# Performance work log

Measured on AMD Instinct MI355X. Metric: run time of the kernel, lower is better.

Reference implementation:

```python
import jax, jax.numpy as jnp
import numpy as np

HEADS = 8
DIM_HEAD = 32
HTK = 576
WTK = 576


def layernorm(x, g, b, eps=1e-6):
    mu = x.mean(-1, keepdims=True)
    var = ((x - mu) ** 2).mean(-1, keepdims=True)
    return (x - mu) * jax.lax.rsqrt(var + eps) * g + b


def conv2d(x, w, b, pad, groups=1):
    y = jax.lax.conv_general_dilated(
        x, w, (1, 1), [(pad, pad), (pad, pad)],
        dimension_numbers=('NCHW', 'OIHW', 'NCHW'),
        feature_group_count=groups)
    return y + b[None, :, None, None]


def prune_attn(attn, htk, wtk):
    B, H, N, _ = attn.shape
    bi = jnp.arange(B)[:, None, None]
    hi = jnp.arange(H)[None, :, None]
    # row pruning: score rows by mean over keys, keep top-k rows
    row_scores = attn.mean(-1)                       # [B,H,N]
    _, top_row = jax.lax.top_k(row_scores, htk)      # [B,H,htk]
    row_mask = jnp.zeros((B, H, N), attn.dtype).at[bi, hi, top_row].set(1.0)
    # col pruning: score cols by mean over queries, keep top-k cols
    col_scores = attn.mean(-2)                       # [B,H,N]
    _, top_col = jax.lax.top_k(col_scores, wtk)
    col_mask = jnp.zeros((B, H, N), attn.dtype).at[bi, hi, top_col].set(1.0)
    return attn * row_mask[..., :, None] * col_mask[..., None, :]


def setup_inputs() -> dict:
    key = jax.random.key(0)
    ks = jax.random.split(key, 24)
    C = 256
    hid = C * 4
    g = C // 8
    s = 0.02
    inp = {
        'x': jax.random.normal(ks[0], (2, C, 48, 48), jnp.float32),
        'qkv_w': jax.random.normal(ks[1], (C, 3 * C), jnp.float32) * s,
        'out_w': jax.random.normal(ks[2], (C, C), jnp.float32) * s,
        'ln1_g': jnp.ones((C,), jnp.float32),
        'ln1_b': jnp.zeros((C,), jnp.float32),
        'ln2_g': jnp.ones((C,), jnp.float32),
        'ln2_b': jnp.zeros((C,), jnp.float32),
        'dw_w': jax.random.normal(ks[3], (C, 1, 3, 3), jnp.float32) * s,
        'dw_b': jnp.zeros((C,), jnp.float32),
        'pw_w': jax.random.normal(ks[4], (C, C, 1, 1), jnp.float32) * s,
        'pw_b': jnp.zeros((C,), jnp.float32),
        'sg1_w': jax.random.normal(ks[5], (g, C, 1, 1), jnp.float32) * s,
        'sg1_b': jnp.zeros((g,), jnp.float32),
        'sg2_w': jax.random.normal(ks[6], (1, g, 7, 7), jnp.float32) * s,
        'sg2_b': jnp.zeros((1,), jnp.float32),
        'cg1_w': jax.random.normal(ks[7], (g, C, 1, 1), jnp.float32) * s,
        'cg1_b': jnp.zeros((g,), jnp.float32),
        'cg2_w': jax.random.normal(ks[8], (C, g, 1, 1), jnp.float32) * s,
        'cg2_b': jnp.zeros((C,), jnp.float32),
        'ff_w1': jax.random.normal(ks[9], (C, hid), jnp.float32) * s,
        'ff_b1': jnp.zeros((hid,), jnp.float32),
        'ff_w2': jax.random.normal(ks[10], (hid, C), jnp.float32) * s,
        'ff_b2': jnp.zeros((C,), jnp.float32),
        'gamma1': jnp.full((1,), 0.5, jnp.float32),
        'gamma2': jnp.full((1,), 0.5, jnp.float32),
    }
    return inp


def reference(x, qkv_w, out_w, ln1_g, ln1_b, ln2_g, ln2_b, dw_w, dw_b,
              pw_w, pw_b, sg1_w, sg1_b, sg2_w, sg2_b, cg1_w, cg1_b,
              cg2_w, cg2_b, ff_w1, ff_b1, ff_w2, ff_b2, gamma1, gamma2):
    B, C, H, W = x.shape
    N = H * W
    # ---- dual-pruned self-attention branch ----
    xa = x.transpose(0, 2, 3, 1).reshape(B, N, C)
    xa = layernorm(xa, ln1_g, ln1_b)
    qkv = xa @ qkv_w                                    # [B,N,3C]
    q, k, v = jnp.split(qkv, 3, axis=-1)
    rs = lambda t: t.reshape(B, N, HEADS, DIM_HEAD).transpose(0, 2, 1, 3)
    q, k, v = rs(q), rs(k), rs(v)                       # [B,h,N,d]
    attn = jnp.einsum('bhid,bhjd->bhij', q, k) * (DIM_HEAD ** -0.5)
    attn = prune_attn(attn, HTK, WTK)
    attn = jax.nn.softmax(attn, axis=-1)
    o = jnp.einsum('bhij,bhjd->bhid', attn, v)
    o = o.transpose(0, 2, 1, 3).reshape(B, N, C) @ out_w
    x_attn = o.reshape(B, H, W, C).transpose(0, 3, 1, 2)
    # ---- conv branch ----
    xc = conv2d(x, dw_w, dw_b, pad=1, groups=C)
    xc = conv2d(xc, pw_w, pw_b, pad=0)
    xs = x_attn + xc
    # ---- gates ----
    sg = jax.nn.silu(conv2d(xs, sg1_w, sg1_b, pad=0))
    sg = jax.nn.sigmoid(conv2d(sg, sg2_w, sg2_b, pad=3))   # [B,1,H,W]
    cg = xs.mean(axis=(2, 3), keepdims=True)                # [B,C,1,1]
    cg = jax.nn.silu(conv2d(cg, cg1_w, cg1_b, pad=0))
    cg = jax.nn.sigmoid(conv2d(cg, cg2_w, cg2_b, pad=0))
    x2 = x + gamma1[0] * (xs * sg * cg)
    # ---- FFN ----
    normed = layernorm(x2.transpose(0, 2, 3, 1), ln2_g, ln2_b)
    h = jax.nn.gelu(normed @ ff_w1 + ff_b1, approximate=False)
    ff = (h @ ff_w2 + ff_b2).transpose(0, 3, 1, 2)
    return x2 + gamma2[0] * ff
```

## Files before the change

kernel.cpp:

```cpp
#include <hip/hip_runtime.h>
#include <math.h>

#define N_PIX 2304
#define CCH   256
#define BHN   16
#define KTOP  576
#define NROWS 4608

typedef unsigned short u16;
typedef __attribute__((ext_vector_type(8))) short short8v;
typedef __attribute__((ext_vector_type(4))) float floatx4;

__device__ __forceinline__ u16 f2b(float f) {
  unsigned int u = __float_as_uint(f);
  return (u16)((u + 0x7fffu + ((u >> 16) & 1u)) >> 16);
}
__device__ __forceinline__ float b2f(u16 v) {
  return __uint_as_float(((unsigned int)v) << 16);
}

__device__ __forceinline__ void async16(const void* g, void* l) {
  __builtin_amdgcn_global_load_lds(
      (const __attribute__((address_space(1))) unsigned int*)g,
      (__attribute__((address_space(3))) unsigned int*)l, 16, 0, 0);
}

__device__ __forceinline__ float erf_apx(float x) {
  float ax = fabsf(x);
  float u = 1.f / (1.f + 0.3275911f * ax);
  float y = u * (0.254829592f + u * (-0.284496736f + u * (1.421413741f +
            u * (-1.453152027f + u * 1.061405429f))));
  float r = 1.f - y * expf(-ax * ax);
  return (x < 0.f) ? -r : r;
}

__global__ __launch_bounds__(256) void lncast_kernel(
    const float* __restrict__ x, u16* __restrict__ xa_bf, float* __restrict__ xnhwc,
    const float* __restrict__ g, const float* __restrict__ beta,
    const float* __restrict__ qkv_w, const float* __restrict__ out_w,
    const float* __restrict__ pw_w, const float* __restrict__ ff_w1,
    const float* __restrict__ ff_w2, const float* __restrict__ sg1_w,
    u16* __restrict__ qkvBT, u16* __restrict__ outBT, u16* __restrict__ pwBT,
    u16* __restrict__ ff1BT, u16* __restrict__ ff2BT, u16* __restrict__ sg1BT)
{
  __shared__ float tile[32 * 257];
  __shared__ float redS[8 * 32], redQ[8 * 32];
  __shared__ float mu_s[32], rs_s[32];
  int tid = threadIdx.x;
  if (blockIdx.x >= 144) {
    int i = (blockIdx.x - 144) * 256 + tid;
    if (i < 196608) { int k = i / 768, n = i - k * 768; qkvBT[n * 256 + k] = f2b(qkv_w[i]); return; }
    i -= 196608;
    if (i < 65536) { int k = i >> 8, n = i & 255; outBT[n * 256 + k] = f2b(out_w[i]); return; }
    i -= 65536;
    if (i < 65536) { pwBT[i] = f2b(pw_w[i]); return; }
    i -= 65536;
    if (i < 262144) { int k = i >> 10, n = i & 1023; ff1BT[n * 256 + k] = f2b(ff_w1[i]); return; }
    i -= 262144;
    if (i < 262144) { int k = i & 1023, n = i >> 10; ff2BT[i] = f2b(ff_w2[k * 256 + n]); return; }
    i -= 262144;
    if (i < 16384) sg1BT[i] = (i < 8192) ? f2b(sg1_w[i]) : (u16)0;
    return;
  }
  int p0g = blockIdx.x * 32;
  int bb = p0g / N_PIX; int p0 = p0g - bb * N_PIX;
  int px = tid & 31, csub = tid >> 5;
  float sacc = 0.f, qacc = 0.f;
#pragma unroll 4
  for (int it = 0; it < 32; ++it) {
    int c = it * 8 + csub;
    float v = x[((long)bb * 256 + c) * N_PIX + p0 + px];
    tile[px * 257 + c] = v;
    sacc += v; qacc += v * v;
  }
  redS[csub * 32 + px] = sacc; redQ[csub * 32 + px] = qacc;
  __syncthreads();
  if (tid < 32) {
    float s = 0.f, qq = 0.f;
#pragma unroll
    for (int j = 0; j < 8; ++j) { s += redS[j * 32 + tid]; qq += redQ[j * 32 + tid]; }
    float mu = s * (1.f / 256.f);
    float var = qq * (1.f / 256.f) - mu * mu;
    mu_s[tid] = mu; rs_s[tid] = rsqrtf(var + 1e-6f);
  }
  __syncthreads();
  float gv = g[tid], bv = beta[tid];
#pragma unroll 4
  for (int it = 0; it < 32; ++it) {
    float v = tile[it * 257 + tid];
    long orow = (long)(p0g + it) * 256 + tid;
    xnhwc[orow] = v;
    xa_bf[orow] = f2b((v - mu_s[it]) * rs_s[it] * gv + bv);
  }
}

template<int MT, int EPI, int CS>
__global__ __launch_bounds__(256) void mgemm(
    const u16* __restrict__ A, const u16* __restrict__ BT,
    float* __restrict__ C, u16* __restrict__ C2,
    int K, int ldc, int nvalid,
    const float* __restrict__ bias, const float* __restrict__ add,
    const float* __restrict__ gamma,
    float* __restrict__ cs_out, int cs_ld)
{
  __shared__ u16 Als[MT * 64 * 32];
  __shared__ u16 Bls[64 * 32];
  int tid = threadIdx.x;
  int w = tid >> 6, lane = tid & 63;
  int row0 = blockIdx.y * (MT * 64), col0 = blockIdx.x * 64;
  const u16* Abase = A + (long)row0 * K;
  const u16* Bbase = BT + (long)col0 * K;
  int q = lane >> 4, l15 = lane & 15;

  floatx4 acc[MT][4];
#pragma unroll
  for (int mi = 0; mi < MT; ++mi)
#pragma unroll
    for (int ni = 0; ni < 4; ++ni) acc[mi][ni] = (floatx4)0.f;

  int ccB = w * 64 + lane;
  int rB = ccB >> 2, kB = (ccB & 3) << 3;

  for (int k0 = 0; k0 < K; k0 += 32) {
#pragma unroll
    for (int i = 0; i < MT; ++i) {
      int cc = w * (64 * MT) + i * 64 + lane;
      async16(Abase + (long)(cc >> 2) * K + k0 + ((cc & 3) << 3), &Als[cc * 8]);
    }
    async16(Bbase + (long)rB * K + k0 + kB, &Bls[ccB * 8]);
    __syncthreads();
    short8v a[MT];
#pragma unroll
    for (int mi = 0; mi < MT; ++mi)
      a[mi] = *(const short8v*)&Als[(w * (16 * MT) + mi * 16 + l15) * 32 + q * 8];
#pragma unroll
    for (int ni = 0; ni < 4; ++ni) {
      short8v b = *(const short8v*)&Bls[(ni * 16 + l15) * 32 + q * 8];
#pragma unroll
      for (int mi = 0; mi < MT; ++mi)
        acc[mi][ni] = __builtin_amdgcn_mfma_f32_16x16x32_bf16(a[mi], b, acc[mi][ni], 0, 0, 0);
    }
    __syncthreads();
  }

  float g2 = (EPI == 5) ? gamma[0] : 0.f;
  float cp[4] = {0.f, 0.f, 0.f, 0.f};
#pragma unroll
  for (int mi = 0; mi < MT; ++mi) {
#pragma unroll
    for (int ni = 0; ni < 4; ++ni) {
      int c = col0 + ni * 16 + l15;
      int rbase = row0 + w * (16 * MT) + mi * 16 + q * 4;
#pragma unroll
      for (int reg = 0; reg < 4; ++reg) {
        long row = rbase + reg;
        float v = acc[mi][ni][reg];
        if (EPI == 0) {
          C[row * ldc + c] = v;
          if (CS) cp[ni] += v;
        } else if (EPI == 3) {
          if (c < nvalid) {
            float t = v + bias[c];
            C[row * (long)nvalid + c] = t / (1.f + expf(-t));
          }
        } else if (EPI == 4) {
          float t = v + bias[c];
          t = 0.5f * t * (1.f + erf_apx(t * 0.70710678f));
          C2[row * ldc + c] = f2b(t);
        } else if (EPI == 5) {
          float t = add[row * 256 + c] + g2 * (v + bias[c]);
          int bb = (int)(row / N_PIX); int p = (int)(row - (long)bb * N_PIX);
          C[((long)bb * 256 + c) * N_PIX + p] = t;
        } else if (EPI == 6) {
          float t = v + bias[c] + add[row * ldc + c];
          C2[row * ldc + c] = f2b(t);
          if (CS) cp[ni] += t;
        }
      }
    }
  }
  if (CS) {
    int bb = (row0 >= N_PIX) ? 1 : 0;
#pragma unroll
    for (int ni = 0; ni < 4; ++ni) {
      float r = cp[ni];
      r += __shfl_xor(r, 16);
      r += __shfl_xor(r, 32);
      if (lane < 16) atomicAdd(&cs_out[bb * cs_ld + col0 + ni * 16 + l15], r);
    }
  }
}

__global__ __launch_bounds__(256) void topkscore_kernel(
    const float* __restrict__ qkv, const float* __restrict__ csum, int* __restrict__ out_idx)
{
  int bh = blockIdx.x, which = blockIdx.y;
  int b = bh >> 3, h = bh & 7;
  int* out = out_idx + (which * BHN + bh) * KTOP;
  __shared__ unsigned int u[N_PIX];
  __shared__ unsigned int hist[256];
  __shared__ unsigned int wtmp[4];
  __shared__ unsigned int sh_selbin, sh_selS;
  __shared__ unsigned int cnt_eq[4], cnt_sel[4];
  __shared__ float svl[32];
  int tid = threadIdx.x;
  int wave = tid >> 6, lane = tid & 63;
  unsigned long long ltmask = (1ull << lane) - 1ull;
  if (tid < 32) svl[tid] = csum[b * 768 + (which ? 0 : 256) + h * 32 + tid];
  __syncthreads();
  int off = (which ? 256 : 0) + h * 32;
  for (int i = tid; i < N_PIX; i += 256) {
    const float4* p4 = (const float4*)(qkv + ((long)(b * N_PIX + i)) * 768 + off);
    float sc = 0.f;
#pragma unroll
    for (int j = 0; j < 8; ++j) {
      float4 v = p4[j];
      sc += v.x * svl[j * 4] + v.y * svl[j * 4 + 1] + v.z * svl[j * 4 + 2] + v.w * svl[j * 4 + 3];
    }
    unsigned int bu = __float_as_uint(sc);
    u[i] = (bu & 0x80000000u) ? ~bu : (bu | 0x80000000u);
  }
  __syncthreads();
  unsigned int prefix = 0u, kRem = KTOP;
  for (int pass = 0; pass < 4; ++pass) {
    int shift = 24 - pass * 8;
    hist[tid] = 0u;
    __syncthreads();
    unsigned int mask = (pass == 0) ? 0u : (0xFFFFFFFFu << (shift + 8));
    for (int i = tid; i < N_PIX; i += 256) {
      unsigned int v = u[i];
      if ((v & mask) == prefix) atomicAdd(&hist[(v >> shift) & 255u], 1u);
    }
    __syncthreads();
    int v = (int)hist[255 - tid];
    int xsc = v;
#pragma unroll
    for (int o = 1; o < 64; o <<= 1) { int y = __shfl_up(xsc, o); if (lane >= o) xsc += y; }
    if (lane == 63) wtmp[wave] = (unsigned int)xsc;
    __syncthreads();
    int wadd = 0;
    for (int ww = 0; ww < wave; ++ww) wadd += (int)wtmp[ww];
    unsigned int S = (unsigned int)(xsc + wadd - v);
    if (S < kRem && S + (unsigned int)v >= kRem) { sh_selbin = (unsigned int)(255 - tid); sh_selS = S; }
    __syncthreads();
    prefix |= (sh_selbin << shift);
    kRem -= sh_selS;
    __syncthreads();
  }
  unsigned int T = prefix;
  unsigned int run_sel = 0u, run_eq = 0u;
  for (int c0 = 0; c0 < N_PIX; c0 += 256) {
    int i = c0 + tid;
    unsigned int v = u[i];
    bool isGt = v > T, isEq = (v == T);
    unsigned long long be = __ballot(isEq);
    unsigned int eqpre = (unsigned int)__popcll(be & ltmask);
    if (lane == 0) cnt_eq[wave] = (unsigned int)__popcll(be);
    __syncthreads();
    unsigned int eqoff = run_eq + eqpre;
    for (int ww = 0; ww < wave; ++ww) eqoff += cnt_eq[ww];
    bool selF = isGt || (isEq && eqoff < kRem);
    unsigned long long bs = __ballot(selF);
    unsigned int spre = (unsigned int)__popcll(bs & ltmask);
    if (lane == 0) cnt_sel[wave] = (unsigned int)__popcll(bs);
    __syncthreads();
    unsigned int soff = run_sel + spre;
    for (int ww = 0; ww < wave; ++ww) soff += cnt_sel[ww];
    if (selF) out[soff] = i;
    unsigned int te = 0, ts = 0;
#pragma unroll
    for (int ww = 0; ww < 4; ++ww) { te += cnt_eq[ww]; ts += cnt_sel[ww]; }
    run_eq += te; run_sel += ts;
    __syncthreads();
  }
}

__global__ __launch_bounds__(256) void gather_kernel(
    const float* __restrict__ qkv, const int* __restrict__ idx,
    u16* __restrict__ Qg, u16* __restrict__ Kg, u16* __restrict__ VgT,
    float* __restrict__ vneg, const float* __restrict__ csum, u16* __restrict__ ofull)
{
  __shared__ float red[256];
  int bh = blockIdx.y;
  int tid = threadIdx.x;
  int r = blockIdx.x * 8 + (tid >> 5);
  int d = tid & 31;
  int b = bh >> 3, h = bh & 7;
  int rn = idx[bh * KTOP + r];
  int cn = idx[(BHN + bh) * KTOP + r];
  const float scale = 0.17677669529663687f;
  float vv = qkv[((long)(b * N_PIX + cn)) * 768 + 512 + h * 32 + d];
  Qg [((long)bh * KTOP + r) * 32 + d] = f2b(qkv[((long)(b * N_PIX + rn)) * 768 + h * 32 + d] * scale);
  Kg [((long)bh * KTOP + r) * 32 + d] = f2b(qkv[((long)(b * N_PIX + cn)) * 768 + 256 + h * 32 + d]);
  VgT[((long)bh * 32 + d) * 584 + r] = f2b(vv);
  red[tid] = vv;
  int bid = blockIdx.y * 72 + blockIdx.x;
  int row = 4 * bid + (tid >> 6);
  int b2 = row / N_PIX;
  int c4 = (tid & 63) * 4;
  const float* vm = csum + b2 * 768 + 512 + c4;
  ushort4 ov;
  ov.x = f2b(vm[0] * (1.f / (float)N_PIX));
  ov.y = f2b(vm[1] * (1.f / (float)N_PIX));
  ov.z = f2b(vm[2] * (1.f / (float)N_PIX));
  ov.w = f2b(vm[3] * (1.f / (float)N_PIX));
  *(ushort4*)&ofull[(long)row * 256 + c4] = ov;
  __syncthreads();
  if (tid < 32) {
    float s = 0.f;
#pragma unroll
    for (int j = 0; j < 8; ++j) s += red[j * 32 + tid];
    atomicAdd(&vneg[bh * 32 + tid], s);
  }
}

__global__ __launch_bounds__(256) void attn_kernel(
    const u16* __restrict__ Qg, const u16* __restrict__ Kg, const u16* __restrict__ VgT,
    const float* __restrict__ csum, const float* __restrict__ vneg,
    const int* __restrict__ idx, u16* __restrict__ ofull)
{
  __shared__ u16 Pls[32 * 584];
  __shared__ float wmax[4 * 32], wsum[4 * 32];
  __shared__ float emv_s[32], invd_s[32], vdif_s[32];
  int bh = blockIdx.y;
  int row0 = blockIdx.x * 32;
  int tid = threadIdx.x;
  int w = tid >> 6, lane = tid & 63;
  int q = lane >> 4, l15 = lane & 15;
  int b = bh >> 3, h = bh & 7;
  if (tid < 32) vdif_s[tid] = csum[b * 768 + 512 + h * 32 + tid] - vneg[bh * 32 + tid];
  const u16* Qb = Qg + (long)bh * KTOP * 32;
  const u16* Kb = Kg + (long)bh * KTOP * 32;
  short8v af[2];
#pragma unroll
  for (int mi = 0; mi < 2; ++mi)
    af[mi] = *(const short8v*)(Qb + ((long)(row0 + mi * 16 + l15)) * 32 + q * 8);
  floatx4 sacc[2][9];
#pragma unroll
  for (int mi = 0; mi < 2; ++mi)
#pragma unroll
    for (int ni = 0; ni < 9; ++ni) sacc[mi][ni] = (floatx4)0.f;
#pragma unroll
  for (int ni = 0; ni < 9; ++ni) {
    int n = w * 144 + ni * 16 + l15;
    short8v bf = *(const short8v*)(Kb + (long)n * 32 + q * 8);
#pragma unroll
    for (int mi = 0; mi < 2; ++mi)
      sacc[mi][ni] = __builtin_amdgcn_mfma_f32_16x16x32_bf16(af[mi], bf, sacc[mi][ni], 0, 0, 0);
  }
#pragma unroll
  for (int mi = 0; mi < 2; ++mi)
#pragma unroll
    for (int reg = 0; reg < 4; ++reg) {
      float m = sacc[mi][0][reg];
#pragma unroll
      for (int ni = 1; ni < 9; ++ni) m = fmaxf(m, sacc[mi][ni][reg]);
#pragma unroll
      for (int o = 1; o < 16; o <<= 1) m = fmaxf(m, __shfl_xor(m, o));
      if (l15 == 0) wmax[w * 32 + mi * 16 + q * 4 + reg] = m;
    }
  __syncthreads();
#pragma unroll
  for (int mi = 0; mi < 2; ++mi)
#pragma unroll
    for (int reg = 0; reg < 4; ++reg) {
      int r = mi * 16 + q * 4 + reg;
      float gm = fmaxf(fmaxf(fmaxf(wmax[r], wmax[32 + r]), fmaxf(wmax[64 + r], wmax[96 + r])), 0.f);
      float s = 0.f;
#pragma unroll
      for (int ni = 0; ni < 9; ++ni) {
        float e = expf(sacc[mi][ni][reg] - gm);
        s += e;
        Pls[r * 584 + w * 144 + ni * 16 + l15] = f2b(e);
      }
#pragma unroll
      for (int o = 1; o < 16; o <<= 1) s += __shfl_xor(s, o);
      if (l15 == 0) wsum[w * 32 + r] = s;
    }
  __syncthreads();
  if (tid < 32) {
    float gm = fmaxf(fmaxf(fmaxf(wmax[tid], wmax[32 + tid]), fmaxf(wmax[64 + tid], wmax[96 + tid])), 0.f);
    float s = wsum[tid] + wsum[32 + tid] + wsum[64 + tid] + wsum[96 + tid];
    float em = expf(-gm);
    float inv = 1.f / (s + (float)(N_PIX - KTOP) * em);
    invd_s[tid] = inv;
    emv_s[tid] = em * inv;
  }
  __syncthreads();
  int mw = w & 1, nw = w >> 1;
  const u16* Vb = VgT + (long)bh * 32 * 584;
  floatx4 acc = (floatx4)0.f;
#pragma unroll
  for (int kt = 0; kt < 18; ++kt) {
    int k0 = kt * 32;
    short8v a = *(const short8v*)&Pls[(mw * 16 + l15) * 584 + k0 + q * 8];
    short8v bb = *(const short8v*)(Vb + (long)(nw * 16 + l15) * 584 + k0 + q * 8);
    acc = __builtin_amdgcn_mfma_f32_16x16x32_bf16(a, bb, acc, 0, 0, 0);
  }
  int d = nw * 16 + l15;
  float vd = vdif_s[d];
#pragma unroll
  for (int reg = 0; reg < 4; ++reg) {
    int r = mw * 16 + q * 4 + reg;
    float o = acc[reg] * invd_s[r] + emv_s[r] * vd;
    int n = idx[bh * KTOP + row0 + r];
    ofull[((long)(b * N_PIX + n)) * 256 + h * 32 + d] = f2b(o);
  }
}

__global__ __launch_bounds__(256) void dwconv_kernel(
    const float* __restrict__ xnhwc, const float* __restrict__ w,
    const float* __restrict__ bias, u16* __restrict__ out_nhwc)
{
  int pix = blockIdx.x;
  int b = pix / N_PIX; int p = pix - b * N_PIX;
  int y = p / 48, xx = p - y * 48;
  int c = threadIdx.x;
  float acc = bias[c];
#pragma unroll
  for (int ky = 0; ky < 3; ++ky) {
    int yy = y + ky - 1; if (yy < 0 || yy >= 48) continue;
#pragma unroll
    for (int kx = 0; kx < 3; ++kx) {
      int xc = xx + kx - 1; if (xc < 0 || xc >= 48) continue;
      acc += w[c * 9 + ky * 3 + kx] * xnhwc[((long)(b * N_PIX + yy * 48 + xc)) * 256 + c];
    }
  }
  out_nhwc[(long)pix * 256 + c] = f2b(acc);
}

__global__ __launch_bounds__(256) void sgcg_kernel(
    const float* __restrict__ sga, const float* __restrict__ w,
    const float* __restrict__ b1, float* __restrict__ sgate,
    const float* __restrict__ cgm, const float* __restrict__ cw1, const float* __restrict__ cb1,
    const float* __restrict__ cw2, const float* __restrict__ cb2, float* __restrict__ cgate)
{
  __shared__ float ws[32 * 49];
  __shared__ float red[4 * 64];
  __shared__ float m[256];
  __shared__ float a[32];
  int t = threadIdx.x;
  if (blockIdx.x >= 96) {
    int b = blockIdx.x - 96;
    m[t] = cgm[b * 256 + t] * (1.f / (float)N_PIX);
    __syncthreads();
    if (t < 32) {
      float s = cb1[t];
      for (int c = 0; c < 256; ++c) s += cw1[t * 256 + c] * m[c];
      a[t] = s / (1.f + expf(-s));
    }
    __syncthreads();
    float s = cb2[t];
#pragma unroll
    for (int g = 0; g < 32; ++g) s += cw2[t * 32 + g] * a[g];
    cgate[b * 256 + t] = 1.f / (1.f + expf(-s));
    return;
  }
  int by = blockIdx.x; int b = by / 48, y = by - b * 48;
  for (int i = t; i < 32 * 49; i += 256) ws[i] = w[i];
  __syncthreads();
  int xx = t & 63, gg = t >> 6;
  float acc = 0.f;
  if (xx < 48) {
    for (int ky = 0; ky < 7; ++ky) {
      int yy = y + ky - 3; if (yy < 0 || yy >= 48) continue;
      for (int kx = 0; kx < 7; ++kx) {
        int xc = xx + kx - 3; if (xc < 0 || xc >= 48) continue;
        const float4* sp = (const float4*)(sga + ((long)(b * N_PIX + yy * 48 + xc)) * 32 + gg * 8);
        float4 v0 = sp[0], v1 = sp[1];
        int wb = gg * 8 * 49 + ky * 7 + kx;
        acc += ws[wb] * v0.x + ws[wb + 49] * v0.y + ws[wb + 98] * v0.z + ws[wb + 147] * v0.w;
        acc += ws[wb + 196] * v1.x + ws[wb + 245] * v1.y + ws[wb + 294] * v1.z + ws[wb + 343] * v1.w;
      }
    }
  }
  red[gg * 64 + xx] = acc;
  __syncthreads();
  if (t < 48) {
    float tot = b1[0] + red[t] + red[64 + t] + red[128 + t] + red[192 + t];
    sgate[b * N_PIX + y * 48 + t] = 1.f / (1.f + expf(-tot));
  }
}

__global__ __launch_bounds__(256) void x2ln_kernel(
    const float* __restrict__ xnhwc, const u16* __restrict__ xs_bf,
    const float* __restrict__ sgate, const float* __restrict__ cgate,
    const float* __restrict__ gamma1, float* __restrict__ x2,
    const float* __restrict__ g, const float* __restrict__ bvec, u16* __restrict__ normed)
{
  __shared__ float red[256];
  int pix = blockIdx.x; int b = pix / N_PIX;
  int c = threadIdx.x;
  float xsv = b2f(xs_bf[(long)pix * 256 + c]);
  float v = xnhwc[(long)pix * 256 + c] + gamma1[0] * xsv * sgate[pix] * cgate[b * 256 + c];
  x2[(long)pix * 256 + c] = v;
  red[c] = v; __syncthreads();
  for (int off = 128; off > 0; off >>= 1) { if (c < off) red[c] += red[c + off]; __syncthreads(); }
  float mu = red[0] * (1.f / 256.f);
  __syncthreads();
  float dv = v - mu;
  red[c] = dv * dv; __syncthreads();
  for (int off = 128; off > 0; off >>= 1) { if (c < off) red[c] += red[c + off]; __syncthreads(); }
  float var = red[0] * (1.f / 256.f);
  normed[(long)pix * 256 + c] = f2b(dv * rsqrtf(var + 1e-6f) * g[c] + bvec[c]);
}

extern "C" void kernel_launch(void* const* d_in, const int* in_sizes, int n_in,
                              void* d_out, int out_size, void* d_ws, size_t ws_size,
                              hipStream_t stream) {
  (void)in_sizes; (void)n_in; (void)out_size; (void)ws_size;
  const float* x      = (const float*)d_in[0];
  const float* qkv_w  = (const float*)d_in[1];
  const float* out_w  = (const float*)d_in[2];
  const float* ln1_g  = (const float*)d_in[3];
  const float* ln1_b  = (const float*)d_in[4];
  const float* ln2_g  = (const float*)d_in[5];
  const float* ln2_b  = (const float*)d_in[6];
  const float* dw_w   = (const float*)d_in[7];
  const float* dw_b   = (const float*)d_in[8];
  const float* pw_w   = (const float*)d_in[9];
  const float* pw_b   = (const float*)d_in[10];
  const float* sg1_w  = (const float*)d_in[11];
  const float* sg1_b  = (const float*)d_in[12];
  const float* sg2_w  = (const float*)d_in[13];
  const float* sg2_b  = (const float*)d_in[14];
  const float* cg1_w  = (const float*)d_in[15];
  const float* cg1_b  = (const float*)d_in[16];
  const float* cg2_w  = (const float*)d_in[17];
  const float* cg2_b  = (const float*)d_in[18];
  const float* ff_w1  = (const float*)d_in[19];
  const float* ff_b1  = (const float*)d_in[20];
  const float* ff_w2  = (const float*)d_in[21];
  const float* ff_b2  = (const float*)d_in[22];
  const float* gamma1 = (const float*)d_in[23];
  const float* gamma2 = (const float*)d_in[24];
  float* out = (float*)d_out;
  float* ws  = (float*)d_ws;

  float* qkv     = ws + 0;
  float* attn_out= ws + 3538944;
  float* x2      = ws + 4718592;
  float* xnhwc   = ws + 5898240;
  u16*   ofull_bf= (u16*)(ws + 7077888);
  u16*   xa_bf   = (u16*)(ws + 7667712);
  u16*   xs_bf   = (u16*)(ws + 8257536);
  u16*   Qg_bf   = (u16*)(ws + 8847360);
  u16*   Kg_bf   = (u16*)(ws + 8994816);
  u16*   VgT     = (u16*)(ws + 9142272);
  float* sga     = ws + 9291776;
  float* csum    = ws + 9439232;
  float* vneg    = ws + 9440768;
  float* cgm     = ws + 9441280;
  float* sgate   = ws + 9441792;
  float* cgate   = ws + 9446400;
  int*   idxb    = (int*)(ws + 9446912);
  u16*   qkvBT   = (u16*)(ws + 9465344);
  u16*   outBT   = (u16*)(ws + 9563648);
  u16*   pwBT    = (u16*)(ws + 9596416);
  u16*   ff1BT   = (u16*)(ws + 9629184);
  u16*   ff2BT   = (u16*)(ws + 9760256);
  u16*   sg1BT   = (u16*)(ws + 9891328);
  u16*   h_bf     = (u16*)qkv;
  u16*   normed_bf= (u16*)(ws + 2359296);
  u16*   dwc_bf   = xa_bf;

  dim3 blk(256);
  hipMemsetAsync(csum, 0, 2560 * sizeof(float), stream);

  lncast_kernel<<<dim3(3536), blk, 0, stream>>>(x, xa_bf, xnhwc, ln1_g, ln1_b,
      qkv_w, out_w, pw_w, ff_w1, ff_w2, sg1_w,
      qkvBT, outBT, pwBT, ff1BT, ff2BT, sg1BT);

  mgemm<2, 0, 1><<<dim3(12, 36), blk, 0, stream>>>(xa_bf, qkvBT, qkv, nullptr,
      256, 768, 768, nullptr, nullptr, nullptr, csum, 768);
  topkscore_kernel<<<dim3(BHN, 2), blk, 0, stream>>>(qkv, csum, idxb);
  gather_kernel<<<dim3(72, BHN), blk, 0, stream>>>(qkv, idxb, Qg_bf, Kg_bf, VgT, vneg,
      csum, ofull_bf);
  attn_kernel<<<dim3(18, BHN), blk, 0, stream>>>(Qg_bf, Kg_bf, VgT, csum, vneg, idxb, ofull_bf);
  mgemm<1, 0, 0><<<dim3(4, 72), blk, 0, stream>>>(ofull_bf, outBT, attn_out, nullptr,
      256, 256, 256, nullptr, nullptr, nullptr, nullptr, 0);

  dwconv_kernel<<<dim3(NROWS), blk, 0, stream>>>(xnhwc, dw_w, dw_b, dwc_bf);
  mgemm<1, 6, 1><<<dim3(4, 72), blk, 0, stream>>>(dwc_bf, pwBT, nullptr, xs_bf,
      256, 256, 256, pw_b, attn_out, nullptr, cgm, 256);

  mgemm<1, 3, 0><<<dim3(1, 72), blk, 0, stream>>>(xs_bf, sg1BT, sga, nullptr,
      256, 32, 32, sg1_b, nullptr, nullptr, nullptr, 0);
  sgcg_kernel<<<dim3(98), blk, 0, stream>>>(sga, sg2_w, sg2_b, sgate,
      cgm, cg1_w, cg1_b, cg2_w, cg2_b, cgate);

  x2ln_kernel<<<dim3(NROWS), blk, 0, stream>>>(xnhwc, xs_bf, sgate, cgate, gamma1, x2,
      ln2_g, ln2_b, normed_bf);

  mgemm<2, 4, 0><<<dim3(16, 36), blk, 0, stream>>>(normed_bf, ff1BT, nullptr, h_bf,
      256, 1024, 1024, ff_b1, nullptr, nullptr, nullptr, 0);
  mgemm<1, 5, 0><<<dim3(4, 72), blk, 0, stream>>>(h_bf, ff2BT, out, nullptr,
      1024, 256, 256, ff_b2, x2, gamma2, nullptr, 0);
}
```

Measured before the change: 257.1 us.

## Fuse out-projection and pointwise conv into one K=512 GEMM; recompute x2 in FFN epilogue

Attention output and depthwise-conv output are now written side by side into one 512-wide bf16 buffer, and the out_w and pw_w weights are concatenated. A single GEMM then computes attn@out_w + dwc@pw_w + bias, which removes a separate GEMM launch and the fp32 attn_out round trip. The x2 residual is no longer stored by the layernorm kernel; the final FFN GEMM epilogue recomputes it from xnhwc, xs, sgate and cgate. The epilogue therefore does more reads per element, including an extra bf16 xs load.

```diff
diff --git a/kernel.cpp b/kernel.cpp
--- a/kernel.cpp
+++ b/kernel.cpp
@@ -40,7 +40,7 @@
     const float* __restrict__ qkv_w, const float* __restrict__ out_w,
     const float* __restrict__ pw_w, const float* __restrict__ ff_w1,
     const float* __restrict__ ff_w2, const float* __restrict__ sg1_w,
-    u16* __restrict__ qkvBT, u16* __restrict__ outBT, u16* __restrict__ pwBT,
+    u16* __restrict__ qkvBT, u16* __restrict__ B2,
     u16* __restrict__ ff1BT, u16* __restrict__ ff2BT, u16* __restrict__ sg1BT)
 {
   __shared__ float tile[32 * 257];
@@ -51,9 +51,9 @@
     int i = (blockIdx.x - 144) * 256 + tid;
     if (i < 196608) { int k = i / 768, n = i - k * 768; qkvBT[n * 256 + k] = f2b(qkv_w[i]); return; }
     i -= 196608;
-    if (i < 65536) { int k = i >> 8, n = i & 255; outBT[n * 256 + k] = f2b(out_w[i]); return; }
+    if (i < 65536) { int k = i >> 8, n = i & 255; B2[n * 512 + k] = f2b(out_w[i]); return; }
     i -= 65536;
-    if (i < 65536) { pwBT[i] = f2b(pw_w[i]); return; }
+    if (i < 65536) { int n = i >> 8, ic = i & 255; B2[n * 512 + 256 + ic] = f2b(pw_w[i]); return; }
     i -= 65536;
     if (i < 262144) { int k = i >> 10, n = i & 1023; ff1BT[n * 256 + k] = f2b(ff_w1[i]); return; }
     i -= 262144;
@@ -101,7 +101,9 @@
     int K, int ldc, int nvalid,
     const float* __restrict__ bias, const float* __restrict__ add,
     const float* __restrict__ gamma,
-    float* __restrict__ cs_out, int cs_ld)
+    float* __restrict__ cs_out, int cs_ld,
+    const u16* __restrict__ xs2, const float* __restrict__ sgv,
+    const float* __restrict__ cgv, const float* __restrict__ g1p)
 {
   __shared__ u16 Als[MT * 64 * 32];
   __shared__ u16 Bls[64 * 32];
@@ -144,6 +146,7 @@
   }
 
   float g2 = (EPI == 5) ? gamma[0] : 0.f;
+  float g1v = (EPI == 5) ? g1p[0] : 0.f;
   float cp[4] = {0.f, 0.f, 0.f, 0.f};
 #pragma unroll
   for (int mi = 0; mi < MT; ++mi) {
@@ -168,11 +171,13 @@
           t = 0.5f * t * (1.f + erf_apx(t * 0.70710678f));
           C2[row * ldc + c] = f2b(t);
         } else if (EPI == 5) {
-          float t = add[row * 256 + c] + g2 * (v + bias[c]);
           int bb = (int)(row / N_PIX); int p = (int)(row - (long)bb * N_PIX);
+          float xsv = b2f(xs2[row * 256 + c]);
+          float x2v = add[row * 256 + c] + g1v * xsv * sgv[row] * cgv[bb * 256 + c];
+          float t = x2v + g2 * (v + bias[c]);
           C[((long)bb * 256 + c) * N_PIX + p] = t;
-        } else if (EPI == 6) {
-          float t = v + bias[c] + add[row * ldc + c];
+        } else if (EPI == 7) {
+          float t = v + bias[c];
           C2[row * ldc + c] = f2b(t);
           if (CS) cp[ni] += t;
         }
@@ -278,7 +283,7 @@
 __global__ __launch_bounds__(256) void gather_kernel(
     const float* __restrict__ qkv, const int* __restrict__ idx,
     u16* __restrict__ Qg, u16* __restrict__ Kg, u16* __restrict__ VgT,
-    float* __restrict__ vneg, const float* __restrict__ csum, u16* __restrict__ ofull)
+    float* __restrict__ vneg, const float* __restrict__ csum, u16* __restrict__ A2)
 {
   __shared__ float red[256];
   int bh = blockIdx.y;
@@ -304,7 +309,7 @@
   ov.y = f2b(vm[1] * (1.f / (float)N_PIX));
   ov.z = f2b(vm[2] * (1.f / (float)N_PIX));
   ov.w = f2b(vm[3] * (1.f / (float)N_PIX));
-  *(ushort4*)&ofull[(long)row * 256 + c4] = ov;
+  *(ushort4*)&A2[(long)row * 512 + c4] = ov;
   __syncthreads();
   if (tid < 32) {
     float s = 0.f;
@@ -317,7 +322,7 @@
 __global__ __launch_bounds__(256) void attn_kernel(
     const u16* __restrict__ Qg, const u16* __restrict__ Kg, const u16* __restrict__ VgT,
     const float* __restrict__ csum, const float* __restrict__ vneg,
-    const int* __restrict__ idx, u16* __restrict__ ofull)
+    const int* __restrict__ idx, u16* __restrict__ A2)
 {
   __shared__ u16 Pls[32 * 584];
   __shared__ float wmax[4 * 32], wsum[4 * 32];
@@ -404,13 +409,13 @@
     int r = mw * 16 + q * 4 + reg;
     float o = acc[reg] * invd_s[r] + emv_s[r] * vd;
     int n = idx[bh * KTOP + row0 + r];
-    ofull[((long)(b * N_PIX + n)) * 256 + h * 32 + d] = f2b(o);
+    A2[((long)(b * N_PIX + n)) * 512 + h * 32 + d] = f2b(o);
   }
 }
 
 __global__ __launch_bounds__(256) void dwconv_kernel(
     const float* __restrict__ xnhwc, const float* __restrict__ w,
-    const float* __restrict__ bias, u16* __restrict__ out_nhwc)
+    const float* __restrict__ bias, u16* __restrict__ A2)
 {
   int pix = blockIdx.x;
   int b = pix / N_PIX; int p = pix - b * N_PIX;
@@ -426,7 +431,7 @@
       acc += w[c * 9 + ky * 3 + kx] * xnhwc[((long)(b * N_PIX + yy * 48 + xc)) * 256 + c];
     }
   }
-  out_nhwc[(long)pix * 256 + c] = f2b(acc);
+  A2[(long)pix * 512 + 256 + c] = f2b(acc);
 }
 
 __global__ __launch_bounds__(256) void sgcg_kernel(
@@ -482,10 +487,10 @@
   }
 }
 
-__global__ __launch_bounds__(256) void x2ln_kernel(
+__global__ __launch_bounds__(256) void gln_kernel(
     const float* __restrict__ xnhwc, const u16* __restrict__ xs_bf,
     const float* __restrict__ sgate, const float* __restrict__ cgate,
-    const float* __restrict__ gamma1, float* __restrict__ x2,
+    const float* __restrict__ gamma1,
     const float* __restrict__ g, const float* __restrict__ bvec, u16* __restrict__ normed)
 {
   __shared__ float red[256];
@@ -493,7 +498,6 @@
   int c = threadIdx.x;
   float xsv = b2f(xs_bf[(long)pix * 256 + c]);
   float v = xnhwc[(long)pix * 256 + c] + gamma1[0] * xsv * sgate[pix] * cgate[b * 256 + c];
-  x2[(long)pix * 256 + c] = v;
   red[c] = v; __syncthreads();
   for (int off = 128; off > 0; off >>= 1) { if (c < off) red[c] += red[c + off]; __syncthreads(); }
   float mu = red[0] * (1.f / 256.f);
@@ -538,62 +542,57 @@
   float* ws  = (float*)d_ws;
 
   float* qkv     = ws + 0;
-  float* attn_out= ws + 3538944;
-  float* x2      = ws + 4718592;
-  float* xnhwc   = ws + 5898240;
-  u16*   ofull_bf= (u16*)(ws + 7077888);
-  u16*   xa_bf   = (u16*)(ws + 7667712);
-  u16*   xs_bf   = (u16*)(ws + 8257536);
-  u16*   Qg_bf   = (u16*)(ws + 8847360);
-  u16*   Kg_bf   = (u16*)(ws + 8994816);
-  u16*   VgT     = (u16*)(ws + 9142272);
-  float* sga     = ws + 9291776;
-  float* csum    = ws + 9439232;
-  float* vneg    = ws + 9440768;
-  float* cgm     = ws + 9441280;
-  float* sgate   = ws + 9441792;
-  float* cgate   = ws + 9446400;
-  int*   idxb    = (int*)(ws + 9446912);
-  u16*   qkvBT   = (u16*)(ws + 9465344);
-  u16*   outBT   = (u16*)(ws + 9563648);
-  u16*   pwBT    = (u16*)(ws + 9596416);
-  u16*   ff1BT   = (u16*)(ws + 9629184);
-  u16*   ff2BT   = (u16*)(ws + 9760256);
-  u16*   sg1BT   = (u16*)(ws + 9891328);
+  u16*   A2      = (u16*)(ws + 3538944);
+  float* xnhwc   = ws + 4718592;
+  u16*   xa_bf   = (u16*)(ws + 5898240);
+  u16*   xs_bf   = (u16*)(ws + 6488064);
+  u16*   Qg_bf   = (u16*)(ws + 7077888);
+  u16*   Kg_bf   = (u16*)(ws + 7225344);
+  u16*   VgT     = (u16*)(ws + 7372800);
+  float* sga     = ws + 7522304;
+  float* csum    = ws + 7669760;
+  float* vneg    = ws + 7671296;
+  float* cgm     = ws + 7671808;
+  float* sgate   = ws + 7672320;
+  float* cgate   = ws + 7676928;
+  int*   idxb    = (int*)(ws + 7677440);
+  u16*   qkvBT   = (u16*)(ws + 7695872);
+  u16*   B2combo = (u16*)(ws + 7794176);
+  u16*   ff1BT   = (u16*)(ws + 7859712);
+  u16*   ff2BT   = (u16*)(ws + 7990784);
+  u16*   sg1BT   = (u16*)(ws + 8121856);
   u16*   h_bf     = (u16*)qkv;
   u16*   normed_bf= (u16*)(ws + 2359296);
-  u16*   dwc_bf   = xa_bf;
 
   dim3 blk(256);
   hipMemsetAsync(csum, 0, 2560 * sizeof(float), stream);
 
   lncast_kernel<<<dim3(3536), blk, 0, stream>>>(x, xa_bf, xnhwc, ln1_g, ln1_b,
       qkv_w, out_w, pw_w, ff_w1, ff_w2, sg1_w,
-      qkvBT, outBT, pwBT, ff1BT, ff2BT, sg1BT);
+      qkvBT, B2combo, ff1BT, ff2BT, sg1BT);
 
   mgemm<2, 0, 1><<<dim3(12, 36), blk, 0, stream>>>(xa_bf, qkvBT, qkv, nullptr,
-      256, 768, 768, nullptr, nullptr, nullptr, csum, 768);
+      256, 768, 768, nullptr, nullptr, nullptr, csum, 768, nullptr, nullptr, nullptr, nullptr);
   topkscore_kernel<<<dim3(BHN, 2), blk, 0, stream>>>(qkv, csum, idxb);
   gather_kernel<<<dim3(72, BHN), blk, 0, stream>>>(qkv, idxb, Qg_bf, Kg_bf, VgT, vneg,
-      csum, ofull_bf);
-  attn_kernel<<<dim3(18, BHN), blk, 0, stream>>>(Qg_bf, Kg_bf, VgT, csum, vneg, idxb, ofull_bf);
-  mgemm<1, 0, 0><<<dim3(4, 72), blk, 0, stream>>>(ofull_bf, outBT, attn_out, nullptr,
-      256, 256, 256, nullptr, nullptr, nullptr, nullptr, 0);
-
-  dwconv_kernel<<<dim3(NROWS), blk, 0, stream>>>(xnhwc, dw_w, dw_b, dwc_bf);
-  mgemm<1, 6, 1><<<dim3(4, 72), blk, 0, stream>>>(dwc_bf, pwBT, nullptr, xs_bf,
-      256, 256, 256, pw_b, attn_out, nullptr, cgm, 256);
+      csum, A2);
+  attn_kernel<<<dim3(18, BHN), blk, 0, stream>>>(Qg_bf, Kg_bf, VgT, csum, vneg, idxb, A2);
+
+  dwconv_kernel<<<dim3(NROWS), blk, 0, stream>>>(xnhwc, dw_w, dw_b, A2);
+
+  mgemm<1, 7, 1><<<dim3(4, 72), blk, 0, stream>>>(A2, B2combo, nullptr, xs_bf,
+      512, 256, 256, pw_b, nullptr, nullptr, cgm, 256, nullptr, nullptr, nullptr, nullptr);
 
   mgemm<1, 3, 0><<<dim3(1, 72), blk, 0, stream>>>(xs_bf, sg1BT, sga, nullptr,
-      256, 32, 32, sg1_b, nullptr, nullptr, nullptr, 0);
+      256, 32, 32, sg1_b, nullptr, nullptr, nullptr, 0, nullptr, nullptr, nullptr, nullptr);
   sgcg_kernel<<<dim3(98), blk, 0, stream>>>(sga, sg2_w, sg2_b, sgate,
       cgm, cg1_w, cg1_b, cg2_w, cg2_b, cgate);
 
-  x2ln_kernel<<<dim3(NROWS), blk, 0, stream>>>(xnhwc, xs_bf, sgate, cgate, gamma1, x2,
+  gln_kernel<<<dim3(NROWS), blk, 0, stream>>>(xnhwc, xs_bf, sgate, cgate, gamma1,
       ln2_g, ln2_b, normed_bf);
 
   mgemm<2, 4, 0><<<dim3(16, 36), blk, 0, stream>>>(normed_bf, ff1BT, nullptr, h_bf,
-      256, 1024, 1024, ff_b1, nullptr, nullptr, nullptr, 0);
+      256, 1024, 1024, ff_b1, nullptr, nullptr, nullptr, 0, nullptr, nullptr, nullptr, nullptr);
   mgemm<1, 5, 0><<<dim3(4, 72), blk, 0, stream>>>(h_bf, ff2BT, out, nullptr,
-      1024, 256, 256, ff_b2, x2, gamma2, nullptr, 0);
-}
+      1024, 256, 256, ff_b2, xnhwc, gamma2, nullptr, 0, xs_bf, sgate, cgate, gamma1);
+}
```

Measured after the change: 256.7 us. About the same (-0.2%).
